# Kernel optimization log

Measured on AMD Instinct MI355X. Metric: run time of the kernel, lower is better.

The kernel has to match this reference:

```python
import jax, jax.numpy as jnp
import numpy as np
import math

M, D = 512, 512          # memory_size, feature_dim
B, H, W = 16, 64, 64     # conv feature map
TEMP_UPDATE, TEMP_GATHER = 0.1, 0.1


def _l2norm(x, axis):
    # torch F.normalize: x / clamp(||x||, min=eps)
    return x / jnp.maximum(jnp.linalg.norm(x, axis=axis, keepdims=True), 1e-12)


def setup_inputs() -> dict:
    key = jax.random.key(0)
    k1, k2 = jax.random.split(key)
    return {
        "query": jax.random.normal(k1, (B, D, H, W), jnp.float32),
        "keys": jax.random.normal(k2, (M, D), jnp.float32),
    }


def reference(query, keys):
    b, d, h, w = query.shape
    m = keys.shape[0]
    # L2-normalize over channel dim, then [b,h,w,d] -> flatten to [N,d]
    qn = _l2norm(query, 1)
    q = jnp.transpose(qn, (0, 2, 3, 1)).reshape(-1, d)  # [N, d]

    scale = math.sqrt(d) * max(TEMP_GATHER, 1e-6)
    logits = (q @ keys.T) / scale                       # [N, M]
    score_q = jax.nn.softmax(logits, axis=0)            # softmax over queries
    score_m = jax.nn.softmax(logits, axis=1)            # softmax over memory slots

    # ---- gather_loss (train) ----
    _, idx2 = jax.lax.top_k(score_m, 2)                 # [N, 2]
    pos = jax.lax.stop_gradient(keys[idx2[:, 0]])       # top-1 slot
    neg = jax.lax.stop_gradient(keys[idx2[:, 1]])       # top-2 slot (hard negative)
    compactness_loss = jnp.mean((q - pos) ** 2)
    # torch TripletMarginLoss(margin=1.0): pairwise_distance adds eps=1e-6 to diff
    dpos = jnp.linalg.norm(q - pos + 1e-6, axis=1)
    dneg = jnp.linalg.norm(q - neg + 1e-6, axis=1)
    separateness_loss = jnp.mean(jax.nn.relu(dpos - dneg + 1.0))

    # ---- read ----
    concat_mem = jax.lax.stop_gradient(score_m) @ keys  # [N, d]
    updated_query = jnp.concatenate([q, concat_mem], axis=1).reshape(b, h, w, 2 * d)
    updated_query = jnp.transpose(updated_query, (0, 3, 1, 2))  # [b, 2d, h, w]

    # ---- update (torch.no_grad) ----
    g = idx2[:, 0]                                              # gathering indices [N]
    wgt = jnp.take_along_axis(score_q, g[:, None], axis=1)[:, 0]
    query_update = jax.ops.segment_sum(q * wgt[:, None], g, num_segments=m)  # scatter-add
    mmt = min(max(1.0 / max(TEMP_UPDATE, 1e-6), 0.0), 0.999)
    updated_memory = _l2norm(keys * mmt + query_update * (1.0 - mmt), 1)
    updated_memory = jax.lax.stop_gradient(updated_memory)

    return (updated_query, updated_memory, score_q, score_m,
            separateness_loss, compactness_loss)
```

## Files before the change

### kernel.cpp

```cpp
#include <hip/hip_runtime.h>
#include <stdint.h>

#define UM_OFF   67108864u
#define SQ_OFF   67371008u
#define SM_OFF   100925440u
#define SEP_OFF  134479872u
#define COMP_OFF 134479873u

#define WS_QBF   0u
#define WS_EBF   67108864u
#define WS_KBF   134217728u
#define WS_KTBF  134742016u
#define WS_W     135266304u
#define WS_RSUM  135528448u
#define WS_CSUM  135790592u
#define WS_KN2   135792640u
#define WS_KSM   135794688u
#define WS_CNT   135796736u
#define WS_QSUM  135798784u
#define WS_LIST  136060928u

typedef __attribute__((ext_vector_type(8))) short short8v;
typedef __attribute__((ext_vector_type(4))) float float4v;

__device__ __forceinline__ unsigned short f2bf(float f) {
  union { float f; uint32_t u; } v; v.f = f;
  return (unsigned short)((v.u + 0x7fffu + ((v.u >> 16) & 1u)) >> 16);
}
__device__ __forceinline__ float bf2f(unsigned short s) {
  union { uint32_t u; float f; } v; v.u = ((uint32_t)s) << 16;
  return v.f;
}

#define GLDS16(gp, lp) __builtin_amdgcn_global_load_lds( \
    (__attribute__((address_space(1))) const void*)(gp), \
    (__attribute__((address_space(3))) void*)(lp), 16, 0, 0)

__global__ __launch_bounds__(512) void k01_prep_norm(
    const float* __restrict__ query, const float* __restrict__ keys,
    unsigned short* __restrict__ kbf, unsigned short* __restrict__ ktbf,
    float* __restrict__ csum, float* __restrict__ rsum,
    float* __restrict__ kn2, float* __restrict__ ksm, int* __restrict__ cnt,
    unsigned short* __restrict__ qbf, float* __restrict__ qsum,
    float* __restrict__ out) {
  int tid = threadIdx.x;
  if (blockIdx.x >= 1024) {
    __shared__ float pn[8], ps[8];
    int b = blockIdx.x - 1024;
    int t = tid;
    int i = b * 512 + t;
    float v = keys[i];
    kbf[i] = f2bf(v);
    ktbf[i] = f2bf(keys[(size_t)t * 512 + b]);
    float s1 = v, s2 = v * v;
    #pragma unroll
    for (int off = 1; off < 64; off <<= 1) {
      s1 += __shfl_xor(s1, off);
      s2 += __shfl_xor(s2, off);
    }
    if ((t & 63) == 0) { pn[t >> 6] = s2; ps[t >> 6] = s1; }
    __syncthreads();
    if (t == 0) {
      float n2 = 0.f, sm = 0.f;
      #pragma unroll
      for (int g = 0; g < 8; ++g) { n2 += pn[g]; sm += ps[g]; }
      kn2[b] = n2; ksm[b] = sm;
    }
    if (i < 65536) rsum[i] = 0.0f;
    if (i < 512) { csum[i] = 0.0f; cnt[i] = 0; }
    if (i < 2) out[SEP_OFF + i] = 0.0f;
    return;
  }
  __shared__ unsigned short vals[512 * 65];
  __shared__ float pp[8][64];
  __shared__ float rs[64];
  int bh = blockIdx.x;
  int b = bh >> 6, h = bh & 63;
  int w = tid & 63, dg = tid >> 6;
  const float* src = query + ((size_t)(b * 512) * 64 + h) * 64 + w;
  float ss = 0.f;
  #pragma unroll 4
  for (int i = 0; i < 64; ++i) {
    int d = dg * 64 + i;
    float v = src[(size_t)d * 4096];
    ss += v * v;
    vals[d * 65 + w] = f2bf(v);
  }
  pp[dg][w] = ss;
  __syncthreads();
  if (tid < 64) {
    float s = 0.f;
    #pragma unroll
    for (int g = 0; g < 8; ++g) s += pp[g][tid];
    rs[tid] = 1.0f / fmaxf(sqrtf(s), 1e-12f);
  }
  __syncthreads();
  float rw_ = rs[w];
  float* dst = out + ((size_t)(b * 1024) * 64 + h) * 64 + w;
  #pragma unroll 4
  for (int i = 0; i < 64; ++i) {
    int d = dg * 64 + i;
    __builtin_nontemporal_store(bf2f(vals[d * 65 + w]) * rw_, &dst[(size_t)d * 4096]);
  }
  int w2 = tid >> 3, dc = tid & 7;
  float rw = rs[w2];
  unsigned short* qrow = qbf + ((size_t)bh * 64 + w2) * 512;
  float qs = 0.f;
  #pragma unroll
  for (int g = 0; g < 8; ++g) {
    int d0 = g * 64 + dc * 8;
    short8v pk;
    #pragma unroll
    for (int jj = 0; jj < 8; ++jj) {
      float qn = bf2f(vals[(d0 + jj) * 65 + w2]) * rw;
      qs += qn;
      pk[jj] = (short)f2bf(qn);
    }
    *(short8v*)(qrow + d0) = pk;
  }
  qs += __shfl_xor(qs, 1); qs += __shfl_xor(qs, 2); qs += __shfl_xor(qs, 4);
  if (dc == 0) qsum[bh * 64 + w2] = qs;
}

__global__ __launch_bounds__(256) void k3_gemm1(
    const unsigned short* __restrict__ qbf, const unsigned short* __restrict__ kbf,
    unsigned short* __restrict__ ebf, float* __restrict__ csum, float* __restrict__ rsum) {
  __shared__ unsigned short As[128 * 32];
  __shared__ unsigned short Bs[128 * 32];
  int bid = blockIdx.x;
  int bm = (bid & 7) * 64 + (bid >> 5);
  int bn = (bid >> 3) & 3;
  int tid = threadIdx.x;
  int lane = tid & 63, wid = tid >> 6;
  int wr = wid >> 1, wc = wid & 1;
  float4v acc[4][4];
  #pragma unroll
  for (int m = 0; m < 4; ++m)
    #pragma unroll
    for (int n = 0; n < 4; ++n) acc[m][n] = (float4v){0.f, 0.f, 0.f, 0.f};
  const unsigned short* Abase = qbf + (size_t)bm * 128 * 512;
  const unsigned short* Bbase = kbf + (size_t)bn * 128 * 512;
  int u0 = wid * 128 + lane, u1 = u0 + 64;
  int ra0 = u0 >> 2, ca0 = (u0 & 3) * 8;
  int ra1 = u1 >> 2, ca1 = (u1 & 3) * 8;
  for (int kt = 0; kt < 16; ++kt) {
    const unsigned short* Ak = Abase + kt * 32;
    const unsigned short* Bk = Bbase + kt * 32;
    GLDS16(Ak + (size_t)ra0 * 512 + ca0, &As[(wid * 2 + 0) * 512]);
    GLDS16(Ak + (size_t)ra1 * 512 + ca1, &As[(wid * 2 + 1) * 512]);
    GLDS16(Bk + (size_t)ra0 * 512 + ca0, &Bs[(wid * 2 + 0) * 512]);
    GLDS16(Bk + (size_t)ra1 * 512 + ca1, &Bs[(wid * 2 + 1) * 512]);
    __syncthreads();
    short8v a[4], b[4];
    const unsigned short* pa = As + (wr * 64 + (lane & 15)) * 32 + (lane >> 4) * 8;
    const unsigned short* pb = Bs + (wc * 64 + (lane & 15)) * 32 + (lane >> 4) * 8;
    #pragma unroll
    for (int m = 0; m < 4; ++m) a[m] = *(const short8v*)(pa + m * 512);
    #pragma unroll
    for (int n = 0; n < 4; ++n) b[n] = *(const short8v*)(pb + n * 512);
    #pragma unroll
    for (int m = 0; m < 4; ++m)
      #pragma unroll
      for (int n = 0; n < 4; ++n)
        acc[m][n] = __builtin_amdgcn_mfma_f32_16x16x32_bf16(a[m], b[n], acc[m][n], 0, 0, 0);
    __syncthreads();
  }
  const float inv_scale = 0.44194173824159216f;
  int r0 = bm * 128 + wr * 64 + (lane >> 4) * 4;
  int c0 = bn * 128 + wc * 64 + (lane & 15);
  float cs[4] = {0.f, 0.f, 0.f, 0.f};
  float rp[4][4];
  #pragma unroll
  for (int m = 0; m < 4; ++m)
    #pragma unroll
    for (int j = 0; j < 4; ++j) rp[m][j] = 0.f;
  #pragma unroll
  for (int m = 0; m < 4; ++m)
    #pragma unroll
    for (int n = 0; n < 4; ++n)
      #pragma unroll
      for (int j = 0; j < 4; ++j) {
        float v = __expf(acc[m][n][j] * inv_scale);
        ebf[(size_t)(r0 + m * 16 + j) * 512 + c0 + n * 16] = f2bf(v);
        cs[n] += v;
        rp[m][j] += v;
      }
  #pragma unroll
  for (int n = 0; n < 4; ++n) {
    float v = cs[n];
    v += __shfl_xor(v, 16);
    v += __shfl_xor(v, 32);
    if ((lane >> 4) == 0) atomicAdd(&csum[c0 + n * 16], v);
  }
  #pragma unroll
  for (int m = 0; m < 4; ++m)
    #pragma unroll
    for (int j = 0; j < 4; ++j) {
      float v = rp[m][j];
      v += __shfl_xor(v, 1); v += __shfl_xor(v, 2);
      v += __shfl_xor(v, 4); v += __shfl_xor(v, 8);
      rp[m][j] = v;
    }
  int g16 = lane & 15;
  float myrp = 0.f;
  #pragma unroll
  for (int m = 0; m < 4; ++m)
    #pragma unroll
    for (int j = 0; j < 4; ++j)
      if (g16 == m * 4 + j) myrp = rp[m][j];
  atomicAdd(&rsum[r0 + (g16 >> 2) * 16 + (g16 & 3)], myrp);
}

__global__ __launch_bounds__(256) void k5_fused(
    const unsigned short* __restrict__ ktbf, const unsigned short* __restrict__ ebf,
    const float* __restrict__ rsum, const float* __restrict__ csum,
    const float* __restrict__ qsum, const float* __restrict__ kn2,
    const float* __restrict__ ksm, int* __restrict__ cnt, int* __restrict__ list,
    float* __restrict__ gw, float* __restrict__ out) {
  __shared__ unsigned short As[128 * 32];
  __shared__ unsigned short Bs[128 * 32];
  int bid = blockIdx.x;
  int g = (bid & 7) * 64 + (bid >> 5);
  int b = g >> 5, nt = g & 31, dt = (bid >> 3) & 3;
  int tid = threadIdx.x;
  int lane = tid & 63, wid = tid >> 6;
  int wr = wid >> 1, wc = wid & 1;
  float4v acc[4][4];
  #pragma unroll
  for (int m = 0; m < 4; ++m)
    #pragma unroll
    for (int n = 0; n < 4; ++n) acc[m][n] = (float4v){0.f, 0.f, 0.f, 0.f};
  const unsigned short* Abase = ktbf + (size_t)dt * 128 * 512;
  size_t brow0 = (size_t)g * 128;
  int u0 = wid * 128 + lane, u1 = u0 + 64;
  int ra0 = u0 >> 2, ca0 = (u0 & 3) * 8;
  int ra1 = u1 >> 2, ca1 = (u1 & 3) * 8;
  for (int kt = 0; kt < 16; ++kt) {
    GLDS16(Abase + (size_t)ra0 * 512 + kt * 32 + ca0, &As[(wid * 2 + 0) * 512]);
    GLDS16(Abase + (size_t)ra1 * 512 + kt * 32 + ca1, &As[(wid * 2 + 1) * 512]);
    GLDS16(ebf + (brow0 + ra0) * 512 + kt * 32 + ca0, &Bs[(wid * 2 + 0) * 512]);
    GLDS16(ebf + (brow0 + ra1) * 512 + kt * 32 + ca1, &Bs[(wid * 2 + 1) * 512]);
    __syncthreads();
    short8v a[4], bb[4];
    const unsigned short* pa = As + (wr * 64 + (lane & 15)) * 32 + (lane >> 4) * 8;
    const unsigned short* pb = Bs + (wc * 64 + (lane & 15)) * 32 + (lane >> 4) * 8;
    #pragma unroll
    for (int m = 0; m < 4; ++m) a[m] = *(const short8v*)(pa + m * 512);
    #pragma unroll
    for (int n = 0; n < 4; ++n) bb[n] = *(const short8v*)(pb + n * 512);
    #pragma unroll
    for (int m = 0; m < 4; ++m)
      #pragma unroll
      for (int n = 0; n < 4; ++n)
        acc[m][n] = __builtin_amdgcn_mfma_f32_16x16x32_bf16(a[m], bb[n], acc[m][n], 0, 0, 0);
    __syncthreads();
  }
  {
    float* dst = out + (size_t)b * 4194304 + (size_t)512 * 4096;
    int d0 = dt * 128 + wr * 64 + (lane >> 4) * 4;
    int c0 = nt * 128 + wc * 64 + (lane & 15);
    float invc[4];
    #pragma unroll
    for (int n = 0; n < 4; ++n) invc[n] = 1.0f / rsum[b * 4096 + c0 + n * 16];
    #pragma unroll
    for (int m = 0; m < 4; ++m)
      #pragma unroll
      for (int n = 0; n < 4; ++n)
        #pragma unroll
        for (int j = 0; j < 4; ++j)
          __builtin_nontemporal_store(acc[m][n][j] * invc[n],
              &dst[(size_t)(d0 + m * 16 + j) * 4096 + (c0 + n * 16)]);
  }
  float4v cA = *(const float4v*)(csum + lane * 8);
  float4v cB = *(const float4v*)(csum + lane * 8 + 4);
  float4v rcA, rcB;
  #pragma unroll
  for (int j = 0; j < 4; ++j) { rcA[j] = 1.0f / cA[j]; rcB[j] = 1.0f / cB[j]; }
  float closs = 0.f, sloss = 0.f;
  const float S2 = 4.525483399593904f;
  int r_base = g * 128 + dt * 32 + wid * 8;
  for (int it = 0; it < 8; ++it) {
    int r = r_base + it;
    short8v eb = *(const short8v*)(ebf + (size_t)r * 512 + lane * 8);
    float e[8];
    #pragma unroll
    for (int j = 0; j < 8; ++j) e[j] = bf2f((unsigned short)eb[j]);
    float invr = 1.0f / rsum[r];
    float v1 = -1.f, v2 = -2.f; int i1 = 0, i2 = 0;
    #pragma unroll
    for (int j = 0; j < 8; ++j) {
      float val = e[j]; int idx = lane * 8 + j;
      if (val > v1) { v2 = v1; i2 = i1; v1 = val; i1 = idx; }
      else if (val > v2) { v2 = val; i2 = idx; }
    }
    #pragma unroll
    for (int off = 1; off < 64; off <<= 1) {
      float ov1 = __shfl_xor(v1, off); int oi1 = __shfl_xor(i1, off);
      float ov2 = __shfl_xor(v2, off); int oi2 = __shfl_xor(i2, off);
      bool take = (ov1 > v1) || (ov1 == v1 && oi1 < i1);
      float av = take ? v1 : v2;  int ai = take ? i1 : i2;
      float bv = take ? ov2 : ov1; int bi = take ? oi2 : oi1;
      bool t2 = (bv > av) || (bv == av && bi < ai);
      v2 = t2 ? bv : av; i2 = t2 ? bi : ai;
      v1 = take ? ov1 : v1; i1 = take ? oi1 : i1;
    }
    float* SQrow = out + SQ_OFF + (size_t)r * 512;
    float* SMrow = out + SM_OFF + (size_t)r * 512;
    float4v sq0, sq1, sm0, sm1;
    #pragma unroll
    for (int j = 0; j < 4; ++j) {
      sq0[j] = e[j] * rcA[j];     sq1[j] = e[4 + j] * rcB[j];
      sm0[j] = e[j] * invr;       sm1[j] = e[4 + j] * invr;
    }
    __builtin_nontemporal_store(sq0, (float4v*)(SQrow + lane * 8));
    __builtin_nontemporal_store(sq1, (float4v*)(SQrow + lane * 8 + 4));
    __builtin_nontemporal_store(sm0, (float4v*)(SMrow + lane * 8));
    __builtin_nontemporal_store(sm1, (float4v*)(SMrow + lane * 8 + 4));
    float qs = qsum[r];
    float cp_row = 1.0f + kn2[i1] - S2 * __logf(v1);
    float dp2 = cp_row + 2e-6f * (qs - ksm[i1]) + 5.12e-10f;
    float cn_row = 1.0f + kn2[i2] - S2 * __logf(v2);
    float dn2 = cn_row + 2e-6f * (qs - ksm[i2]) + 5.12e-10f;
    closs += cp_row;
    sloss += fmaxf(sqrtf(dp2) - sqrtf(dn2) + 1.0f, 0.f);
    if (lane == 0) {
      gw[r] = v1 / csum[i1];
      int pos = atomicAdd(&cnt[i1], 1);
      if (pos < 1024) list[(i1 << 10) + pos] = r;
    }
  }
  if (lane == 0) {
    atomicAdd(out + SEP_OFF, sloss * (1.0f / 65536.0f));
    atomicAdd(out + COMP_OFF, closs * (1.0f / (65536.0f * 512.0f)));
  }
}

__global__ __launch_bounds__(512) void k4b_gather(
    const int* __restrict__ cnt, const int* __restrict__ list,
    const float* __restrict__ gw, const unsigned short* __restrict__ qbf,
    const float* __restrict__ keys, float* __restrict__ out) {
  __shared__ float red[8][512];
  __shared__ float wss[8];
  int m = blockIdx.x;
  int tid = threadIdx.x, lane = tid & 63, wid = tid >> 6;
  int n = cnt[m]; if (n > 1024) n = 1024;
  float acc[8] = {0.f, 0.f, 0.f, 0.f, 0.f, 0.f, 0.f, 0.f};
  for (int idx = wid; idx < n; idx += 8) {
    int r = list[(m << 10) + idx];
    float wv = gw[r];
    short8v qv = *(const short8v*)(qbf + (size_t)r * 512 + lane * 8);
    #pragma unroll
    for (int j = 0; j < 8; ++j) acc[j] += wv * bf2f((unsigned short)qv[j]);
  }
  #pragma unroll
  for (int j = 0; j < 8; ++j) red[wid][lane * 8 + j] = acc[j];
  __syncthreads();
  int d0 = tid;
  float s = 0.f;
  #pragma unroll
  for (int g = 0; g < 8; ++g) s += red[g][d0];
  float v = keys[(size_t)m * 512 + d0] * 0.999f + s * 0.001f;
  float ss = v * v;
  #pragma unroll
  for (int off = 1; off < 64; off <<= 1) ss += __shfl_xor(ss, off);
  if (lane == 0) wss[wid] = ss;
  __syncthreads();
  float tot = 0.f;
  #pragma unroll
  for (int g = 0; g < 8; ++g) tot += wss[g];
  float rsn = 1.0f / fmaxf(sqrtf(tot), 1e-12f);
  out[UM_OFF + (size_t)m * 512 + d0] = v * rsn;
}

extern "C" void kernel_launch(void* const* d_in, const int* in_sizes, int n_in,
                              void* d_out, int out_size, void* d_ws, size_t ws_size,
                              hipStream_t stream) {
  const float* query = (const float*)d_in[0];
  const float* keys  = (const float*)d_in[1];
  float* out = (float*)d_out;
  char* ws = (char*)d_ws;
  unsigned short* qbf  = (unsigned short*)(ws + WS_QBF);
  unsigned short* ebf  = (unsigned short*)(ws + WS_EBF);
  unsigned short* kbf  = (unsigned short*)(ws + WS_KBF);
  unsigned short* ktbf = (unsigned short*)(ws + WS_KTBF);
  float* gw   = (float*)(ws + WS_W);
  float* rsum = (float*)(ws + WS_RSUM);
  float* csum = (float*)(ws + WS_CSUM);
  float* kn2  = (float*)(ws + WS_KN2);
  float* ksm  = (float*)(ws + WS_KSM);
  int*   cnt  = (int*)(ws + WS_CNT);
  float* qsum = (float*)(ws + WS_QSUM);
  int*   list = (int*)(ws + WS_LIST);

  k01_prep_norm<<<dim3(1536), dim3(512), 0, stream>>>(
      query, keys, kbf, ktbf, csum, rsum, kn2, ksm, cnt, qbf, qsum, out);
  k3_gemm1<<<dim3(2048), dim3(256), 0, stream>>>(qbf, kbf, ebf, csum, rsum);
  k5_fused<<<dim3(2048), dim3(256), 0, stream>>>(
      ktbf, ebf, rsum, csum, qsum, kn2, ksm, cnt, list, gw, out);
  k4b_gather<<<dim3(512), dim3(512), 0, stream>>>(cnt, list, gw, qbf, keys, out);
}
```

Before: 404.4 us.

## Compute softmax row sums inside the read GEMM and stage exp tile through LDS

The row-sum reduction and its atomics leave the first GEMM. The second GEMM now recomputes each row's sum from the bf16 exp values it already streams through shared memory, and stores them in a small LDS array. The first GEMM also writes its exp tile to a padded LDS buffer and stores it to global memory as coalesced 16-byte rows instead of scattered 2-byte writes. This trades global atomics and a zero-init pass for extra LDS reads and adds inside the main loop. The row sums now come from bf16-rounded values rather than fp32, which shifts precision slightly.

Measured after the change: 415.0 us. 2.6% more time.

```diff
diff --git a/kernel.cpp b/kernel.cpp
--- a/kernel.cpp
+++ b/kernel.cpp
@@ -12,7 +12,6 @@
 #define WS_KBF   134217728u
 #define WS_KTBF  134742016u
 #define WS_W     135266304u
-#define WS_RSUM  135528448u
 #define WS_CSUM  135790592u
 #define WS_KN2   135792640u
 #define WS_KSM   135794688u
@@ -39,7 +38,7 @@
 __global__ __launch_bounds__(512) void k01_prep_norm(
     const float* __restrict__ query, const float* __restrict__ keys,
     unsigned short* __restrict__ kbf, unsigned short* __restrict__ ktbf,
-    float* __restrict__ csum, float* __restrict__ rsum,
+    float* __restrict__ csum,
     float* __restrict__ kn2, float* __restrict__ ksm, int* __restrict__ cnt,
     unsigned short* __restrict__ qbf, float* __restrict__ qsum,
     float* __restrict__ out) {
@@ -66,7 +65,6 @@
       for (int g = 0; g < 8; ++g) { n2 += pn[g]; sm += ps[g]; }
       kn2[b] = n2; ksm[b] = sm;
     }
-    if (i < 65536) rsum[i] = 0.0f;
     if (i < 512) { csum[i] = 0.0f; cnt[i] = 0; }
     if (i < 2) out[SEP_OFF + i] = 0.0f;
     return;
@@ -124,9 +122,10 @@
 
 __global__ __launch_bounds__(256) void k3_gemm1(
     const unsigned short* __restrict__ qbf, const unsigned short* __restrict__ kbf,
-    unsigned short* __restrict__ ebf, float* __restrict__ csum, float* __restrict__ rsum) {
-  __shared__ unsigned short As[128 * 32];
-  __shared__ unsigned short Bs[128 * 32];
+    unsigned short* __restrict__ ebf, float* __restrict__ csum) {
+  __shared__ unsigned short lds[128 * 136];
+  unsigned short* As = lds;
+  unsigned short* Bs = lds + 4096;
   int bid = blockIdx.x;
   int bm = (bid & 7) * 64 + (bid >> 5);
   int bn = (bid >> 3) & 3;
@@ -166,14 +165,9 @@
     __syncthreads();
   }
   const float inv_scale = 0.44194173824159216f;
-  int r0 = bm * 128 + wr * 64 + (lane >> 4) * 4;
-  int c0 = bn * 128 + wc * 64 + (lane & 15);
+  int rl0 = wr * 64 + (lane >> 4) * 4;
+  int cl0 = wc * 64 + (lane & 15);
   float cs[4] = {0.f, 0.f, 0.f, 0.f};
-  float rp[4][4];
-  #pragma unroll
-  for (int m = 0; m < 4; ++m)
-    #pragma unroll
-    for (int j = 0; j < 4; ++j) rp[m][j] = 0.f;
   #pragma unroll
   for (int m = 0; m < 4; ++m)
     #pragma unroll
@@ -181,10 +175,10 @@
       #pragma unroll
       for (int j = 0; j < 4; ++j) {
         float v = __expf(acc[m][n][j] * inv_scale);
-        ebf[(size_t)(r0 + m * 16 + j) * 512 + c0 + n * 16] = f2bf(v);
+        lds[(rl0 + m * 16 + j) * 136 + cl0 + n * 16] = f2bf(v);
         cs[n] += v;
-        rp[m][j] += v;
       }
+  int c0 = bn * 128 + cl0;
   #pragma unroll
   for (int n = 0; n < 4; ++n) {
     float v = cs[n];
@@ -192,33 +186,25 @@
     v += __shfl_xor(v, 32);
     if ((lane >> 4) == 0) atomicAdd(&csum[c0 + n * 16], v);
   }
-  #pragma unroll
-  for (int m = 0; m < 4; ++m)
-    #pragma unroll
-    for (int j = 0; j < 4; ++j) {
-      float v = rp[m][j];
-      v += __shfl_xor(v, 1); v += __shfl_xor(v, 2);
-      v += __shfl_xor(v, 4); v += __shfl_xor(v, 8);
-      rp[m][j] = v;
-    }
-  int g16 = lane & 15;
-  float myrp = 0.f;
-  #pragma unroll
-  for (int m = 0; m < 4; ++m)
-    #pragma unroll
-    for (int j = 0; j < 4; ++j)
-      if (g16 == m * 4 + j) myrp = rp[m][j];
-  atomicAdd(&rsum[r0 + (g16 >> 2) * 16 + (g16 & 3)], myrp);
+  __syncthreads();
+  #pragma unroll
+  for (int i = 0; i < 8; ++i) {
+    int idx = i * 256 + tid;
+    int row = idx >> 4, seg = idx & 15;
+    short8v t8 = *(const short8v*)&lds[row * 136 + seg * 8];
+    *(short8v*)(ebf + (size_t)(bm * 128 + row) * 512 + bn * 128 + seg * 8) = t8;
+  }
 }
 
 __global__ __launch_bounds__(256) void k5_fused(
     const unsigned short* __restrict__ ktbf, const unsigned short* __restrict__ ebf,
-    const float* __restrict__ rsum, const float* __restrict__ csum,
+    const float* __restrict__ csum,
     const float* __restrict__ qsum, const float* __restrict__ kn2,
     const float* __restrict__ ksm, int* __restrict__ cnt, int* __restrict__ list,
     float* __restrict__ gw, float* __restrict__ out) {
   __shared__ unsigned short As[128 * 32];
   __shared__ unsigned short Bs[128 * 32];
+  __shared__ float rs_lds[128];
   int bid = blockIdx.x;
   int g = (bid & 7) * 64 + (bid >> 5);
   int b = g >> 5, nt = g & 31, dt = (bid >> 3) & 3;
@@ -235,6 +221,8 @@
   int u0 = wid * 128 + lane, u1 = u0 + 64;
   int ra0 = u0 >> 2, ca0 = (u0 & 3) * 8;
   int ra1 = u1 >> 2, ca1 = (u1 & 3) * 8;
+  float bsum = 0.f;
+  const unsigned short* prow_sum = Bs + (tid >> 1) * 32 + (tid & 1) * 16;
   for (int kt = 0; kt < 16; ++kt) {
     GLDS16(Abase + (size_t)ra0 * 512 + kt * 32 + ca0, &As[(wid * 2 + 0) * 512]);
     GLDS16(Abase + (size_t)ra1 * 512 + kt * 32 + ca1, &As[(wid * 2 + 1) * 512]);
@@ -253,15 +241,26 @@
       #pragma unroll
       for (int n = 0; n < 4; ++n)
         acc[m][n] = __builtin_amdgcn_mfma_f32_16x16x32_bf16(a[m], bb[n], acc[m][n], 0, 0, 0);
-    __syncthreads();
-  }
+    {
+      short8v x0 = *(const short8v*)(prow_sum);
+      short8v x1 = *(const short8v*)(prow_sum + 8);
+      #pragma unroll
+      for (int j = 0; j < 8; ++j)
+        bsum += bf2f((unsigned short)x0[j]) + bf2f((unsigned short)x1[j]);
+    }
+    __syncthreads();
+  }
+  bsum += __shfl_xor(bsum, 1);
+  if ((tid & 1) == 0) rs_lds[tid >> 1] = bsum;
+  __syncthreads();
   {
     float* dst = out + (size_t)b * 4194304 + (size_t)512 * 4096;
     int d0 = dt * 128 + wr * 64 + (lane >> 4) * 4;
     int c0 = nt * 128 + wc * 64 + (lane & 15);
     float invc[4];
     #pragma unroll
-    for (int n = 0; n < 4; ++n) invc[n] = 1.0f / rsum[b * 4096 + c0 + n * 16];
+    for (int n = 0; n < 4; ++n)
+      invc[n] = 1.0f / rs_lds[wc * 64 + n * 16 + (lane & 15)];
     #pragma unroll
     for (int m = 0; m < 4; ++m)
       #pragma unroll
@@ -285,7 +284,7 @@
     float e[8];
     #pragma unroll
     for (int j = 0; j < 8; ++j) e[j] = bf2f((unsigned short)eb[j]);
-    float invr = 1.0f / rsum[r];
+    float invr = 1.0f / rs_lds[dt * 32 + wid * 8 + it];
     float v1 = -1.f, v2 = -2.f; int i1 = 0, i2 = 0;
     #pragma unroll
     for (int j = 0; j < 8; ++j) {
@@ -384,7 +383,6 @@
   unsigned short* kbf  = (unsigned short*)(ws + WS_KBF);
   unsigned short* ktbf = (unsigned short*)(ws + WS_KTBF);
   float* gw   = (float*)(ws + WS_W);
-  float* rsum = (float*)(ws + WS_RSUM);
   float* csum = (float*)(ws + WS_CSUM);
   float* kn2  = (float*)(ws + WS_KN2);
   float* ksm  = (float*)(ws + WS_KSM);
@@ -393,9 +391,9 @@
   int*   list = (int*)(ws + WS_LIST);
 
   k01_prep_norm<<<dim3(1536), dim3(512), 0, stream>>>(
-      query, keys, kbf, ktbf, csum, rsum, kn2, ksm, cnt, qbf, qsum, out);
-  k3_gemm1<<<dim3(2048), dim3(256), 0, stream>>>(qbf, kbf, ebf, csum, rsum);
+      query, keys, kbf, ktbf, csum, kn2, ksm, cnt, qbf, qsum, out);
+  k3_gemm1<<<dim3(2048), dim3(256), 0, stream>>>(qbf, kbf, ebf, csum);
   k5_fused<<<dim3(2048), dim3(256), 0, stream>>>(
-      ktbf, ebf, rsum, csum, qsum, kn2, ksm, cnt, list, gw, out);
+      ktbf, ebf, csum, qsum, kn2, ksm, cnt, list, gw, out);
   k4b_gather<<<dim3(512), dim3(512), 0, stream>>>(cnt, list, gw, qbf, keys, out);
 }
```
